# Optimization experiments

Measured on AMD Instinct MI355X. Metric: run time of the kernel, lower is better.

Reference implementation:

```python
import jax, jax.numpy as jnp
import numpy as np

EPS = 1e-5
TOP_K = 2


def setup_inputs() -> dict:
    key = jax.random.key(0)
    ks = jax.random.split(key, 6)
    T, H, F, E = 4096, 1024, 2816, 8
    scale = 0.02
    return {
        "hidden_states": jax.random.normal(ks[0], (T, H), dtype=jnp.float32),
        "ln_w": jnp.ones((H,), dtype=jnp.float32),
        "router_w": jax.random.normal(ks[1], (H, E), dtype=jnp.float32) * scale,
        "w_gate": jax.random.normal(ks[2], (E, H, F), dtype=jnp.float32) * scale,
        "w_up": jax.random.normal(ks[3], (E, H, F), dtype=jnp.float32) * scale,
        "w_down": jax.random.normal(ks[4], (E, F, H), dtype=jnp.float32) * scale,
    }


def reference(hidden_states, ln_w, router_w, w_gate, w_up, w_down):
    # RMSNorm (LlamaRMSNorm)
    var = jnp.mean(hidden_states * hidden_states, axis=-1, keepdims=True)
    x = hidden_states * jax.lax.rsqrt(var + EPS) * ln_w  # [T, H]

    # TopKRouter: softmax over experts, then top-k probs/indices
    logits = x @ router_w                     # [T, E]
    probs = jax.nn.softmax(logits, axis=-1)
    topk_p, topk_i = jax.lax.top_k(probs, TOP_K)  # [T, K]

    # Dense combine weights [T, E]: prob for routed experts, 0 otherwise
    T = x.shape[0]
    combine = jnp.zeros_like(probs).at[jnp.arange(T)[:, None], topk_i].add(topk_p)

    # Experts: Llama-style gated MLP (SwiGLU); loop over fixed small expert set
    out = jnp.zeros_like(x)
    for e in range(w_gate.shape[0]):
        h = jax.nn.silu(x @ w_gate[e]) * (x @ w_up[e])   # [T, F]
        out = out + combine[:, e:e + 1] * (h @ w_down[e])
    return out
```

## Files before the change

kernel.cpp:

```cpp
#include <hip/hip_runtime.h>

#define T_TOK 4096
#define H_DIM 1024
#define F_DIM 2816
#define E_NUM 8
#define EPSV 1e-5f

typedef unsigned short u16;
typedef __attribute__((ext_vector_type(8))) short bf16x8;
typedef __attribute__((ext_vector_type(4))) float f32x4;

__device__ __forceinline__ u16 f2bf(float f) {
  union { float f; unsigned u; } c; c.f = f;
  unsigned u = c.u;
  return (u16)((u + 0x7FFFu + ((u >> 16) & 1u)) >> 16);
}

__device__ __forceinline__ void llds16(const u16* g, u16* l) {
  __builtin_amdgcn_global_load_lds(
      (const __attribute__((address_space(1))) unsigned int*)g,
      (__attribute__((address_space(3))) unsigned int*)l, 16, 0, 0);
}

__global__ __launch_bounds__(256) void router_kernel(
    const float* __restrict__ hs, const float* __restrict__ lnw,
    const float* __restrict__ rw, u16* __restrict__ x_h,
    int* __restrict__ cnt, int* __restrict__ list,
    float* __restrict__ wcomb, int* __restrict__ slot) {
  const int wave = threadIdx.x >> 6;
  const int lane = threadIdx.x & 63;
  const int t = blockIdx.x * 4 + wave;
  const float* row = hs + (size_t)t * H_DIM;

  float4 v[4];
  float ss = 0.f;
#pragma unroll
  for (int j = 0; j < 4; ++j) {
    v[j] = ((const float4*)row)[j * 64 + lane];
    ss += v[j].x * v[j].x + v[j].y * v[j].y + v[j].z * v[j].z + v[j].w * v[j].w;
  }
#pragma unroll
  for (int m = 32; m; m >>= 1) ss += __shfl_xor(ss, m, 64);
  const float inv = rsqrtf(ss * (1.0f / H_DIM) + EPSV);

  float lg[E_NUM];
#pragma unroll
  for (int e = 0; e < E_NUM; ++e) lg[e] = 0.f;

#pragma unroll
  for (int j = 0; j < 4; ++j) {
    const int idx = j * 64 + lane;
    const int h0 = idx * 4;
    float4 w4 = ((const float4*)lnw)[idx];
    float xv[4] = {v[j].x * inv * w4.x, v[j].y * inv * w4.y,
                   v[j].z * inv * w4.z, v[j].w * inv * w4.w};
    ushort4 xs;
    xs.x = f2bf(xv[0]); xs.y = f2bf(xv[1]); xs.z = f2bf(xv[2]); xs.w = f2bf(xv[3]);
    ((ushort4*)(x_h + (size_t)t * H_DIM))[idx] = xs;
#pragma unroll
    for (int q = 0; q < 4; ++q) {
      const float* rr = rw + (size_t)(h0 + q) * E_NUM;
      float4 a = ((const float4*)rr)[0];
      float4 b = ((const float4*)rr)[1];
      lg[0] += xv[q] * a.x; lg[1] += xv[q] * a.y;
      lg[2] += xv[q] * a.z; lg[3] += xv[q] * a.w;
      lg[4] += xv[q] * b.x; lg[5] += xv[q] * b.y;
      lg[6] += xv[q] * b.z; lg[7] += xv[q] * b.w;
    }
  }
#pragma unroll
  for (int e = 0; e < E_NUM; ++e)
#pragma unroll
    for (int m = 32; m; m >>= 1) lg[e] += __shfl_xor(lg[e], m, 64);

  if (lane == 0) {
    float mx = lg[0];
#pragma unroll
    for (int e = 1; e < E_NUM; ++e) mx = fmaxf(mx, lg[e]);
    float p[E_NUM], s = 0.f;
#pragma unroll
    for (int e = 0; e < E_NUM; ++e) { p[e] = __expf(lg[e] - mx); s += p[e]; }
    const float invs = 1.0f / s;
    int e1 = 0; float b1 = p[0];
#pragma unroll
    for (int e = 1; e < E_NUM; ++e) if (p[e] > b1) { b1 = p[e]; e1 = e; }
    int e2 = -1; float b2 = -1.f;
#pragma unroll
    for (int e = 0; e < E_NUM; ++e) if (e != e1 && p[e] > b2) { b2 = p[e]; e2 = e; }
    b1 *= invs; b2 *= invs;
    int p1 = atomicAdd(&cnt[e1], 1);
    list[e1 * T_TOK + p1] = t; wcomb[e1 * T_TOK + p1] = b1;
    slot[2 * t] = (e1 << 16) | p1;
    int p2 = atomicAdd(&cnt[e2], 1);
    list[e2 * T_TOK + p2] = t; wcomb[e2 * T_TOK + p2] = b2;
    slot[2 * t + 1] = (e2 << 16) | p2;
  }
}

__global__ void offsets_kernel(const int* __restrict__ cnt, int* __restrict__ offs) {
  if (threadIdx.x == 0) {
    int s = 0;
    for (int e = 0; e < E_NUM; ++e) { offs[e] = s; s += cnt[e]; }
  }
}

__global__ __launch_bounds__(256) void transpose_cvt(
    const float* __restrict__ in, u16* __restrict__ out, int R, int C) {
  __shared__ float tile[32][33];
  const size_t base = (size_t)blockIdx.z * R * C;
  const int c0 = blockIdx.x * 32, r0 = blockIdx.y * 32;
  const int tx = threadIdx.x, ty = threadIdx.y;
#pragma unroll
  for (int j = 0; j < 32; j += 8)
    tile[ty + j][tx] = in[base + (size_t)(r0 + ty + j) * C + c0 + tx];
  __syncthreads();
#pragma unroll
  for (int j = 0; j < 32; j += 8)
    out[base + (size_t)(c0 + ty + j) * R + r0 + tx] = f2bf(tile[tx][ty + j]);
}

__global__ __launch_bounds__(256) void gemm1_kernel(
    const u16* __restrict__ x_h, const u16* __restrict__ wgT,
    const u16* __restrict__ wuT, const int* __restrict__ cnt,
    const int* __restrict__ offs, const int* __restrict__ list,
    u16* __restrict__ hbuf) {
  const int e = blockIdx.z;
  const int n_e = cnt[e];
  const int rt = blockIdx.y;
  if (rt * 128 >= n_e) return;
  const int ft = blockIdx.x;

  __shared__ __align__(16) u16 As[128 * 64];
  __shared__ __align__(16) u16 Bgs[64 * 64];
  __shared__ __align__(16) u16 Bus[64 * 64];
  __shared__ int tok[128];

  const int tid = threadIdx.x;
  if (tid < 128) {
    int r = rt * 128 + tid;
    if (r >= n_e) r = n_e - 1;
    tok[tid] = list[e * T_TOK + r];
  }
  __syncthreads();

  const int wv = tid >> 6, lane = tid & 63;
  const int wm = wv >> 1, wn = wv & 1;
  const int lrow = lane & 15, quad = lane >> 4;
  const int srow = lane >> 3, schunk = lane & 7;

  const u16* agp[4];
#pragma unroll
  for (int i = 0; i < 4; ++i) {
    int r = wv * 32 + i * 8 + srow;
    agp[i] = x_h + (size_t)tok[r] * H_DIM + ((schunk ^ (r & 7)) << 3);
  }
  const size_t wb = ((size_t)e * F_DIM + (size_t)ft * 64) * H_DIM;
  const u16* bgp[2]; const u16* bup[2];
#pragma unroll
  for (int i = 0; i < 2; ++i) {
    int r = wv * 16 + i * 8 + srow;
    size_t g = wb + (size_t)r * H_DIM + ((schunk ^ (r & 7)) << 3);
    bgp[i] = wgT + g;
    bup[i] = wuT + g;
  }

  const u16* aptr[4][2]; const u16* bgptr[2][2]; const u16* buptr[2][2];
#pragma unroll
  for (int tm = 0; tm < 4; ++tm) {
    int row = wm * 64 + tm * 16 + lrow;
#pragma unroll
    for (int ks = 0; ks < 2; ++ks)
      aptr[tm][ks] = &As[row * 64 + (((ks * 4 + quad) ^ (row & 7)) << 3)];
  }
#pragma unroll
  for (int tn = 0; tn < 2; ++tn) {
    int row = wn * 32 + tn * 16 + lrow;
#pragma unroll
    for (int ks = 0; ks < 2; ++ks) {
      int off = row * 64 + (((ks * 4 + quad) ^ (row & 7)) << 3);
      bgptr[tn][ks] = &Bgs[off];
      buptr[tn][ks] = &Bus[off];
    }
  }

  f32x4 accg[4][2], accu[4][2];
#pragma unroll
  for (int i = 0; i < 4; ++i)
#pragma unroll
    for (int j = 0; j < 2; ++j) {
      accg[i][j] = f32x4{0.f, 0.f, 0.f, 0.f};
      accu[i][j] = f32x4{0.f, 0.f, 0.f, 0.f};
    }

  for (int k0 = 0; k0 < H_DIM; k0 += 64) {
#pragma unroll
    for (int i = 0; i < 4; ++i)
      llds16(agp[i] + k0, &As[(wv * 32 + i * 8) * 64]);
#pragma unroll
    for (int i = 0; i < 2; ++i) {
      llds16(bgp[i] + k0, &Bgs[(wv * 16 + i * 8) * 64]);
      llds16(bup[i] + k0, &Bus[(wv * 16 + i * 8) * 64]);
    }
    __syncthreads();
#pragma unroll
    for (int ks = 0; ks < 2; ++ks) {
      bf16x8 a[4], bg[2], bu[2];
#pragma unroll
      for (int tm = 0; tm < 4; ++tm) a[tm] = *(const bf16x8*)aptr[tm][ks];
#pragma unroll
      for (int tn = 0; tn < 2; ++tn) {
        bg[tn] = *(const bf16x8*)bgptr[tn][ks];
        bu[tn] = *(const bf16x8*)buptr[tn][ks];
      }
#pragma unroll
      for (int tm = 0; tm < 4; ++tm)
#pragma unroll
        for (int tn = 0; tn < 2; ++tn) {
          accg[tm][tn] = __builtin_amdgcn_mfma_f32_16x16x32_bf16(a[tm], bg[tn], accg[tm][tn], 0, 0, 0);
          accu[tm][tn] = __builtin_amdgcn_mfma_f32_16x16x32_bf16(a[tm], bu[tn], accu[tm][tn], 0, 0, 0);
        }
    }
    __syncthreads();
  }

  const int oe = offs[e];
#pragma unroll
  for (int tm = 0; tm < 4; ++tm) {
    const int lr0 = wm * 64 + tm * 16 + quad * 4;
#pragma unroll
    for (int rr = 0; rr < 4; ++rr) {
      const int gr = rt * 128 + lr0 + rr;
      if (gr < n_e) {
#pragma unroll
        for (int tn = 0; tn < 2; ++tn) {
          float g = accg[tm][tn][rr];
          float u = accu[tm][tn][rr];
          float hv = g / (1.0f + __expf(-g)) * u;
          int col = ft * 64 + wn * 32 + tn * 16 + lrow;
          hbuf[(size_t)(oe + gr) * F_DIM + col] = f2bf(hv);
        }
      }
    }
  }
}

__global__ __launch_bounds__(256) void gemm2_kernel(
    const u16* __restrict__ hbuf, const u16* __restrict__ wdT,
    const int* __restrict__ cnt, const int* __restrict__ offs,
    const float* __restrict__ wcomb, float* __restrict__ contrib) {
  const int e = blockIdx.z;
  const int n_e = cnt[e];
  const int rt = blockIdx.y;
  if (rt * 128 >= n_e) return;
  const int nt = blockIdx.x;

  __shared__ __align__(16) u16 As[128 * 64];
  __shared__ __align__(16) u16 Bs[128 * 64];
  __shared__ int hrow[128];

  const int tid = threadIdx.x;
  const int oe = offs[e];
  if (tid < 128) {
    int r = rt * 128 + tid;
    if (r >= n_e) r = n_e - 1;
    hrow[tid] = oe + r;
  }
  __syncthreads();

  const int wv = tid >> 6, lane = tid & 63;
  const int wm = wv >> 1, wn = wv & 1;
  const int lrow = lane & 15, quad = lane >> 4;
  const int srow = lane >> 3, schunk = lane & 7;

  const u16* agp[4];
#pragma unroll
  for (int i = 0; i < 4; ++i) {
    int r = wv * 32 + i * 8 + srow;
    agp[i] = hbuf + (size_t)hrow[r] * F_DIM + ((schunk ^ (r & 7)) << 3);
  }
  const size_t wb = ((size_t)e * H_DIM + (size_t)nt * 128) * F_DIM;
  const u16* bgp[4];
#pragma unroll
  for (int i = 0; i < 4; ++i) {
    int r = wv * 32 + i * 8 + srow;
    bgp[i] = wdT + wb + (size_t)r * F_DIM + ((schunk ^ (r & 7)) << 3);
  }

  const u16* aptr[4][2]; const u16* bptr[4][2];
#pragma unroll
  for (int tm = 0; tm < 4; ++tm) {
    int row = wm * 64 + tm * 16 + lrow;
#pragma unroll
    for (int ks = 0; ks < 2; ++ks)
      aptr[tm][ks] = &As[row * 64 + (((ks * 4 + quad) ^ (row & 7)) << 3)];
  }
#pragma unroll
  for (int tn = 0; tn < 4; ++tn) {
    int row = wn * 64 + tn * 16 + lrow;
#pragma unroll
    for (int ks = 0; ks < 2; ++ks)
      bptr[tn][ks] = &Bs[row * 64 + (((ks * 4 + quad) ^ (row & 7)) << 3)];
  }

  f32x4 acc[4][4];
#pragma unroll
  for (int i = 0; i < 4; ++i)
#pragma unroll
    for (int j = 0; j < 4; ++j) acc[i][j] = f32x4{0.f, 0.f, 0.f, 0.f};

  for (int k0 = 0; k0 < F_DIM; k0 += 64) {
#pragma unroll
    for (int i = 0; i < 4; ++i) {
      llds16(agp[i] + k0, &As[(wv * 32 + i * 8) * 64]);
      llds16(bgp[i] + k0, &Bs[(wv * 32 + i * 8) * 64]);
    }
    __syncthreads();
#pragma unroll
    for (int ks = 0; ks < 2; ++ks) {
      bf16x8 a[4], b[4];
#pragma unroll
      for (int tm = 0; tm < 4; ++tm) a[tm] = *(const bf16x8*)aptr[tm][ks];
#pragma unroll
      for (int tn = 0; tn < 4; ++tn) b[tn] = *(const bf16x8*)bptr[tn][ks];
#pragma unroll
      for (int tm = 0; tm < 4; ++tm)
#pragma unroll
        for (int tn = 0; tn < 4; ++tn)
          acc[tm][tn] = __builtin_amdgcn_mfma_f32_16x16x32_bf16(a[tm], b[tn], acc[tm][tn], 0, 0, 0);
    }
    __syncthreads();
  }

#pragma unroll
  for (int tm = 0; tm < 4; ++tm) {
    const int lr0 = wm * 64 + tm * 16 + quad * 4;
#pragma unroll
    for (int rr = 0; rr < 4; ++rr) {
      const int gr = rt * 128 + lr0 + rr;
      if (gr < n_e) {
        const float cw = wcomb[e * T_TOK + gr];
#pragma unroll
        for (int tn = 0; tn < 4; ++tn) {
          int col = nt * 128 + wn * 64 + tn * 16 + lrow;
          contrib[(size_t)(oe + gr) * H_DIM + col] = acc[tm][tn][rr] * cw;
        }
      }
    }
  }
}

__global__ __launch_bounds__(256) void combine_kernel(
    const float* __restrict__ contrib, const int* __restrict__ offs,
    const int* __restrict__ slot, float* __restrict__ out) {
  const int t = blockIdx.x;
  const int s0 = slot[2 * t], s1 = slot[2 * t + 1];
  const int r0 = offs[s0 >> 16] + (s0 & 0xFFFF);
  const int r1 = offs[s1 >> 16] + (s1 & 0xFFFF);
  float4 a = ((const float4*)(contrib + (size_t)r0 * H_DIM))[threadIdx.x];
  float4 b = ((const float4*)(contrib + (size_t)r1 * H_DIM))[threadIdx.x];
  float4 o = {a.x + b.x, a.y + b.y, a.z + b.z, a.w + b.w};
  ((float4*)(out + (size_t)t * H_DIM))[threadIdx.x] = o;
}

extern "C" void kernel_launch(void* const* d_in, const int* in_sizes, int n_in,
                              void* d_out, int out_size, void* d_ws, size_t ws_size,
                              hipStream_t stream) {
  const float* hs  = (const float*)d_in[0];
  const float* lnw = (const float*)d_in[1];
  const float* rw  = (const float*)d_in[2];
  const float* wg  = (const float*)d_in[3];
  const float* wu  = (const float*)d_in[4];
  const float* wd  = (const float*)d_in[5];
  float* out = (float*)d_out;

  char* p = (char*)d_ws;
  const size_t SZ_XH = (size_t)T_TOK * H_DIM * 2;
  const size_t SZ_W  = (size_t)E_NUM * F_DIM * H_DIM * 2;
  const size_t SZ_HB = (size_t)T_TOK * 2 * F_DIM * 2;
  const size_t SZ_CT = (size_t)T_TOK * 2 * H_DIM * 4;

  u16* x_h  = (u16*)p;   p += SZ_XH;
  u16* wgT  = (u16*)p;   p += SZ_W;
  u16* wuT  = (u16*)p;   p += SZ_W;
  u16* wdT  = (u16*)p;   p += SZ_W;
  u16* hbuf = (u16*)p;   p += SZ_HB;
  float* contrib = (float*)p; p += SZ_CT;
  int* cnt  = (int*)p;   p += 256;
  int* offs = (int*)p;   p += 256;
  int* list = (int*)p;   p += (size_t)E_NUM * T_TOK * 4;
  float* wcomb = (float*)p; p += (size_t)E_NUM * T_TOK * 4;
  int* slot = (int*)p;   p += (size_t)T_TOK * 2 * 4;

  hipMemsetAsync(cnt, 0, 256, stream);
  router_kernel<<<T_TOK / 4, 256, 0, stream>>>(hs, lnw, rw, x_h, cnt, list, wcomb, slot);
  offsets_kernel<<<1, 64, 0, stream>>>(cnt, offs);
  transpose_cvt<<<dim3(F_DIM / 32, H_DIM / 32, E_NUM), dim3(32, 8), 0, stream>>>(wg, wgT, H_DIM, F_DIM);
  transpose_cvt<<<dim3(F_DIM / 32, H_DIM / 32, E_NUM), dim3(32, 8), 0, stream>>>(wu, wuT, H_DIM, F_DIM);
  transpose_cvt<<<dim3(H_DIM / 32, F_DIM / 32, E_NUM), dim3(32, 8), 0, stream>>>(wd, wdT, F_DIM, H_DIM);
  gemm1_kernel<<<dim3(F_DIM / 64, T_TOK / 128, E_NUM), 256, 0, stream>>>(x_h, wgT, wuT, cnt, offs, list, hbuf);
  gemm2_kernel<<<dim3(H_DIM / 128, T_TOK / 128, E_NUM), 256, 0, stream>>>(hbuf, wdT, cnt, offs, wcomb, contrib);
  combine_kernel<<<T_TOK, 256, 0, stream>>>(contrib, offs, slot, out);
}
```

Baseline: 652.8 us.

## Double-buffer GEMM LDS loads, fuse weight transposes, atomically scatter expert outputs

Both expert GEMMs now double-buffer their LDS tiles. The next k-slice is issued via global_load_lds before computing the current one, with explicit vmcnt waits and raw barriers, so memory latency overlaps MFMA work. The three weight transpose launches become a single kernel with 128x32 tiles and vectorised float4 reads and ushort4 writes. The contrib buffer and combine kernel are removed: gemm2 atomically adds weighted results directly into a zeroed output. This adds float atomics, whose summation order is nondeterministic, plus a memset of the output. It also doubles LDS use per block, which may lower occupancy.

```diff
diff --git a/kernel.cpp b/kernel.cpp
--- a/kernel.cpp
+++ b/kernel.cpp
@@ -26,7 +26,7 @@
     const float* __restrict__ hs, const float* __restrict__ lnw,
     const float* __restrict__ rw, u16* __restrict__ x_h,
     int* __restrict__ cnt, int* __restrict__ list,
-    float* __restrict__ wcomb, int* __restrict__ slot) {
+    float* __restrict__ wcomb) {
   const int wave = threadIdx.x >> 6;
   const int lane = threadIdx.x & 63;
   const int t = blockIdx.x * 4 + wave;
@@ -90,10 +90,8 @@
     b1 *= invs; b2 *= invs;
     int p1 = atomicAdd(&cnt[e1], 1);
     list[e1 * T_TOK + p1] = t; wcomb[e1 * T_TOK + p1] = b1;
-    slot[2 * t] = (e1 << 16) | p1;
     int p2 = atomicAdd(&cnt[e2], 1);
     list[e2 * T_TOK + p2] = t; wcomb[e2 * T_TOK + p2] = b2;
-    slot[2 * t + 1] = (e2 << 16) | p2;
   }
 }
 
@@ -104,19 +102,46 @@
   }
 }
 
-__global__ __launch_bounds__(256) void transpose_cvt(
-    const float* __restrict__ in, u16* __restrict__ out, int R, int C) {
-  __shared__ float tile[32][33];
-  const size_t base = (size_t)blockIdx.z * R * C;
-  const int c0 = blockIdx.x * 32, r0 = blockIdx.y * 32;
-  const int tx = threadIdx.x, ty = threadIdx.y;
-#pragma unroll
-  for (int j = 0; j < 32; j += 8)
-    tile[ty + j][tx] = in[base + (size_t)(r0 + ty + j) * C + c0 + tx];
+#define TPW 5632
+__global__ __launch_bounds__(256) void transpose_cvt_all(
+    const float* __restrict__ wg, const float* __restrict__ wu,
+    const float* __restrict__ wd, u16* __restrict__ wgT,
+    u16* __restrict__ wuT, u16* __restrict__ wdT) {
+  __shared__ float tile[128][37];
+  const int bx = blockIdx.x;
+  const int which = bx / TPW;
+  const int rem = bx - which * TPW;
+  const int e = rem / 704;
+  const int t = rem - e * 704;
+  const float* in; u16* outp; int R, C, rt, ct;
+  if (which == 0)      { in = wg; outp = wgT; R = H_DIM; C = F_DIM; rt = t / 88; ct = t - rt * 88; }
+  else if (which == 1) { in = wu; outp = wuT; R = H_DIM; C = F_DIM; rt = t / 88; ct = t - rt * 88; }
+  else                 { in = wd; outp = wdT; R = F_DIM; C = H_DIM; rt = t >> 5; ct = t & 31; }
+  const size_t base = (size_t)e * R * C;
+  const int r0 = rt * 128, c0 = ct * 32;
+  const int tid = threadIdx.x;
+
+  const int rr = tid >> 3, cq = tid & 7;
+#pragma unroll
+  for (int i = 0; i < 4; ++i) {
+    float4 v = *(const float4*)(in + base + (size_t)(r0 + rr + 32 * i) * C + c0 + cq * 4);
+    float* dst = &tile[rr + 32 * i][cq * 4];
+    dst[0] = v.x; dst[1] = v.y; dst[2] = v.z; dst[3] = v.w;
+  }
   __syncthreads();
-#pragma unroll
-  for (int j = 0; j < 32; j += 8)
-    out[base + (size_t)(c0 + ty + j) * R + r0 + tx] = f2bf(tile[tx][ty + j]);
+
+  const int cc = tid >> 4, rq0 = tid & 15;
+#pragma unroll
+  for (int jj = 0; jj < 4; ++jj) {
+    const int c = cc + 16 * (jj & 1);
+    const int rq = rq0 + 16 * (jj >> 1);
+    ushort4 o;
+    o.x = f2bf(tile[rq * 4 + 0][c]);
+    o.y = f2bf(tile[rq * 4 + 1][c]);
+    o.z = f2bf(tile[rq * 4 + 2][c]);
+    o.w = f2bf(tile[rq * 4 + 3][c]);
+    *(ushort4*)(outp + base + (size_t)(c0 + c) * R + r0 + rq * 4) = o;
+  }
 }
 
 __global__ __launch_bounds__(256) void gemm1_kernel(
@@ -130,19 +155,11 @@
   if (rt * 128 >= n_e) return;
   const int ft = blockIdx.x;
 
-  __shared__ __align__(16) u16 As[128 * 64];
-  __shared__ __align__(16) u16 Bgs[64 * 64];
-  __shared__ __align__(16) u16 Bus[64 * 64];
-  __shared__ int tok[128];
+  __shared__ __align__(16) u16 As[2][128 * 64];
+  __shared__ __align__(16) u16 Bgs[2][64 * 64];
+  __shared__ __align__(16) u16 Bus[2][64 * 64];
 
   const int tid = threadIdx.x;
-  if (tid < 128) {
-    int r = rt * 128 + tid;
-    if (r >= n_e) r = n_e - 1;
-    tok[tid] = list[e * T_TOK + r];
-  }
-  __syncthreads();
-
   const int wv = tid >> 6, lane = tid & 63;
   const int wm = wv >> 1, wn = wv & 1;
   const int lrow = lane & 15, quad = lane >> 4;
@@ -151,36 +168,35 @@
   const u16* agp[4];
 #pragma unroll
   for (int i = 0; i < 4; ++i) {
-    int r = wv * 32 + i * 8 + srow;
-    agp[i] = x_h + (size_t)tok[r] * H_DIM + ((schunk ^ (r & 7)) << 3);
+    const int rl = wv * 32 + i * 8 + srow;
+    int gr = rt * 128 + rl; if (gr >= n_e) gr = n_e - 1;
+    const int tkn = list[e * T_TOK + gr];
+    agp[i] = x_h + (size_t)tkn * H_DIM + ((schunk ^ (rl & 7)) << 3);
   }
   const size_t wb = ((size_t)e * F_DIM + (size_t)ft * 64) * H_DIM;
   const u16* bgp[2]; const u16* bup[2];
 #pragma unroll
   for (int i = 0; i < 2; ++i) {
-    int r = wv * 16 + i * 8 + srow;
-    size_t g = wb + (size_t)r * H_DIM + ((schunk ^ (r & 7)) << 3);
+    const int r = wv * 16 + i * 8 + srow;
+    const size_t g = wb + (size_t)r * H_DIM + ((schunk ^ (r & 7)) << 3);
     bgp[i] = wgT + g;
     bup[i] = wuT + g;
   }
 
-  const u16* aptr[4][2]; const u16* bgptr[2][2]; const u16* buptr[2][2];
+  int aoff[4][2], boff[2][2];
 #pragma unroll
   for (int tm = 0; tm < 4; ++tm) {
-    int row = wm * 64 + tm * 16 + lrow;
+    const int row = wm * 64 + tm * 16 + lrow;
 #pragma unroll
     for (int ks = 0; ks < 2; ++ks)
-      aptr[tm][ks] = &As[row * 64 + (((ks * 4 + quad) ^ (row & 7)) << 3)];
+      aoff[tm][ks] = row * 64 + (((ks * 4 + quad) ^ (row & 7)) << 3);
   }
 #pragma unroll
   for (int tn = 0; tn < 2; ++tn) {
-    int row = wn * 32 + tn * 16 + lrow;
-#pragma unroll
-    for (int ks = 0; ks < 2; ++ks) {
-      int off = row * 64 + (((ks * 4 + quad) ^ (row & 7)) << 3);
-      bgptr[tn][ks] = &Bgs[off];
-      buptr[tn][ks] = &Bus[off];
-    }
+    const int row = wn * 32 + tn * 16 + lrow;
+#pragma unroll
+    for (int ks = 0; ks < 2; ++ks)
+      boff[tn][ks] = row * 64 + (((ks * 4 + quad) ^ (row & 7)) << 3);
   }
 
   f32x4 accg[4][2], accu[4][2];
@@ -192,25 +208,26 @@
       accu[i][j] = f32x4{0.f, 0.f, 0.f, 0.f};
     }
 
-  for (int k0 = 0; k0 < H_DIM; k0 += 64) {
+  auto stage = [&](int b, int k0) {
 #pragma unroll
     for (int i = 0; i < 4; ++i)
-      llds16(agp[i] + k0, &As[(wv * 32 + i * 8) * 64]);
+      llds16(agp[i] + k0, &As[b][(wv * 32 + i * 8) * 64]);
 #pragma unroll
     for (int i = 0; i < 2; ++i) {
-      llds16(bgp[i] + k0, &Bgs[(wv * 16 + i * 8) * 64]);
-      llds16(bup[i] + k0, &Bus[(wv * 16 + i * 8) * 64]);
-    }
-    __syncthreads();
+      llds16(bgp[i] + k0, &Bgs[b][(wv * 16 + i * 8) * 64]);
+      llds16(bup[i] + k0, &Bus[b][(wv * 16 + i * 8) * 64]);
+    }
+  };
+  auto compute = [&](int b) {
 #pragma unroll
     for (int ks = 0; ks < 2; ++ks) {
       bf16x8 a[4], bg[2], bu[2];
 #pragma unroll
-      for (int tm = 0; tm < 4; ++tm) a[tm] = *(const bf16x8*)aptr[tm][ks];
+      for (int tm = 0; tm < 4; ++tm) a[tm] = *(const bf16x8*)&As[b][aoff[tm][ks]];
 #pragma unroll
       for (int tn = 0; tn < 2; ++tn) {
-        bg[tn] = *(const bf16x8*)bgptr[tn][ks];
-        bu[tn] = *(const bf16x8*)buptr[tn][ks];
+        bg[tn] = *(const bf16x8*)&Bgs[b][boff[tn][ks]];
+        bu[tn] = *(const bf16x8*)&Bus[b][boff[tn][ks]];
       }
 #pragma unroll
       for (int tm = 0; tm < 4; ++tm)
@@ -220,7 +237,31 @@
           accu[tm][tn] = __builtin_amdgcn_mfma_f32_16x16x32_bf16(a[tm], bu[tn], accu[tm][tn], 0, 0, 0);
         }
     }
-    __syncthreads();
+  };
+
+  stage(0, 0);
+#pragma unroll 1
+  for (int k0 = 0; k0 < H_DIM; k0 += 128) {
+    const bool s1 = (k0 + 64) < H_DIM;
+    if (s1) {
+      stage(1, k0 + 64);
+      asm volatile("s_waitcnt vmcnt(8)" ::: "memory");
+    } else {
+      asm volatile("s_waitcnt vmcnt(0)" ::: "memory");
+    }
+    __builtin_amdgcn_s_barrier();
+    compute(0);
+    __builtin_amdgcn_s_barrier();
+    const bool s2 = (k0 + 128) < H_DIM;
+    if (s2) {
+      stage(0, k0 + 128);
+      asm volatile("s_waitcnt vmcnt(8)" ::: "memory");
+    } else {
+      asm volatile("s_waitcnt vmcnt(0)" ::: "memory");
+    }
+    __builtin_amdgcn_s_barrier();
+    compute(1);
+    __builtin_amdgcn_s_barrier();
   }
 
   const int oe = offs[e];
@@ -247,26 +288,19 @@
 __global__ __launch_bounds__(256) void gemm2_kernel(
     const u16* __restrict__ hbuf, const u16* __restrict__ wdT,
     const int* __restrict__ cnt, const int* __restrict__ offs,
-    const float* __restrict__ wcomb, float* __restrict__ contrib) {
+    const float* __restrict__ wcomb, const int* __restrict__ list,
+    float* __restrict__ out) {
   const int e = blockIdx.z;
   const int n_e = cnt[e];
   const int rt = blockIdx.y;
   if (rt * 128 >= n_e) return;
   const int nt = blockIdx.x;
 
-  __shared__ __align__(16) u16 As[128 * 64];
-  __shared__ __align__(16) u16 Bs[128 * 64];
-  __shared__ int hrow[128];
+  __shared__ __align__(16) u16 As[2][128 * 64];
+  __shared__ __align__(16) u16 Bs[2][128 * 64];
 
   const int tid = threadIdx.x;
   const int oe = offs[e];
-  if (tid < 128) {
-    int r = rt * 128 + tid;
-    if (r >= n_e) r = n_e - 1;
-    hrow[tid] = oe + r;
-  }
-  __syncthreads();
-
   const int wv = tid >> 6, lane = tid & 63;
   const int wm = wv >> 1, wn = wv & 1;
   const int lrow = lane & 15, quad = lane >> 4;
@@ -275,31 +309,32 @@
   const u16* agp[4];
 #pragma unroll
   for (int i = 0; i < 4; ++i) {
-    int r = wv * 32 + i * 8 + srow;
-    agp[i] = hbuf + (size_t)hrow[r] * F_DIM + ((schunk ^ (r & 7)) << 3);
+    const int rl = wv * 32 + i * 8 + srow;
+    int gr = rt * 128 + rl; if (gr >= n_e) gr = n_e - 1;
+    agp[i] = hbuf + (size_t)(oe + gr) * F_DIM + ((schunk ^ (rl & 7)) << 3);
   }
   const size_t wb = ((size_t)e * H_DIM + (size_t)nt * 128) * F_DIM;
   const u16* bgp[4];
 #pragma unroll
   for (int i = 0; i < 4; ++i) {
-    int r = wv * 32 + i * 8 + srow;
+    const int r = wv * 32 + i * 8 + srow;
     bgp[i] = wdT + wb + (size_t)r * F_DIM + ((schunk ^ (r & 7)) << 3);
   }
 
-  const u16* aptr[4][2]; const u16* bptr[4][2];
+  int aoff[4][2], boff[4][2];
 #pragma unroll
   for (int tm = 0; tm < 4; ++tm) {
-    int row = wm * 64 + tm * 16 + lrow;
+    const int row = wm * 64 + tm * 16 + lrow;
 #pragma unroll
     for (int ks = 0; ks < 2; ++ks)
-      aptr[tm][ks] = &As[row * 64 + (((ks * 4 + quad) ^ (row & 7)) << 3)];
+      aoff[tm][ks] = row * 64 + (((ks * 4 + quad) ^ (row & 7)) << 3);
   }
 #pragma unroll
   for (int tn = 0; tn < 4; ++tn) {
-    int row = wn * 64 + tn * 16 + lrow;
+    const int row = wn * 64 + tn * 16 + lrow;
 #pragma unroll
     for (int ks = 0; ks < 2; ++ks)
-      bptr[tn][ks] = &Bs[row * 64 + (((ks * 4 + quad) ^ (row & 7)) << 3)];
+      boff[tn][ks] = row * 64 + (((ks * 4 + quad) ^ (row & 7)) << 3);
   }
 
   f32x4 acc[4][4];
@@ -308,27 +343,52 @@
 #pragma unroll
     for (int j = 0; j < 4; ++j) acc[i][j] = f32x4{0.f, 0.f, 0.f, 0.f};
 
-  for (int k0 = 0; k0 < F_DIM; k0 += 64) {
+  auto stage = [&](int b, int k0) {
 #pragma unroll
     for (int i = 0; i < 4; ++i) {
-      llds16(agp[i] + k0, &As[(wv * 32 + i * 8) * 64]);
-      llds16(bgp[i] + k0, &Bs[(wv * 32 + i * 8) * 64]);
-    }
-    __syncthreads();
+      llds16(agp[i] + k0, &As[b][(wv * 32 + i * 8) * 64]);
+      llds16(bgp[i] + k0, &Bs[b][(wv * 32 + i * 8) * 64]);
+    }
+  };
+  auto compute = [&](int b) {
 #pragma unroll
     for (int ks = 0; ks < 2; ++ks) {
-      bf16x8 a[4], b[4];
-#pragma unroll
-      for (int tm = 0; tm < 4; ++tm) a[tm] = *(const bf16x8*)aptr[tm][ks];
-#pragma unroll
-      for (int tn = 0; tn < 4; ++tn) b[tn] = *(const bf16x8*)bptr[tn][ks];
+      bf16x8 a[4], bb[4];
+#pragma unroll
+      for (int tm = 0; tm < 4; ++tm) a[tm] = *(const bf16x8*)&As[b][aoff[tm][ks]];
+#pragma unroll
+      for (int tn = 0; tn < 4; ++tn) bb[tn] = *(const bf16x8*)&Bs[b][boff[tn][ks]];
 #pragma unroll
       for (int tm = 0; tm < 4; ++tm)
 #pragma unroll
         for (int tn = 0; tn < 4; ++tn)
-          acc[tm][tn] = __builtin_amdgcn_mfma_f32_16x16x32_bf16(a[tm], b[tn], acc[tm][tn], 0, 0, 0);
-    }
-    __syncthreads();
+          acc[tm][tn] = __builtin_amdgcn_mfma_f32_16x16x32_bf16(a[tm], bb[tn], acc[tm][tn], 0, 0, 0);
+    }
+  };
+
+  stage(0, 0);
+#pragma unroll 1
+  for (int k0 = 0; k0 < F_DIM; k0 += 128) {
+    const bool s1 = (k0 + 64) < F_DIM;
+    if (s1) {
+      stage(1, k0 + 64);
+      asm volatile("s_waitcnt vmcnt(8)" ::: "memory");
+    } else {
+      asm volatile("s_waitcnt vmcnt(0)" ::: "memory");
+    }
+    __builtin_amdgcn_s_barrier();
+    compute(0);
+    __builtin_amdgcn_s_barrier();
+    const bool s2 = (k0 + 128) < F_DIM;
+    if (s2) {
+      stage(0, k0 + 128);
+      asm volatile("s_waitcnt vmcnt(8)" ::: "memory");
+    } else {
+      asm volatile("s_waitcnt vmcnt(0)" ::: "memory");
+    }
+    __builtin_amdgcn_s_barrier();
+    compute(1);
+    __builtin_amdgcn_s_barrier();
   }
 
 #pragma unroll
@@ -339,27 +399,15 @@
       const int gr = rt * 128 + lr0 + rr;
       if (gr < n_e) {
         const float cw = wcomb[e * T_TOK + gr];
+        const int tkn = list[e * T_TOK + gr];
 #pragma unroll
         for (int tn = 0; tn < 4; ++tn) {
-          int col = nt * 128 + wn * 64 + tn * 16 + lrow;
-          contrib[(size_t)(oe + gr) * H_DIM + col] = acc[tm][tn][rr] * cw;
+          const int col = nt * 128 + wn * 64 + tn * 16 + lrow;
+          atomicAdd(&out[(size_t)tkn * H_DIM + col], acc[tm][tn][rr] * cw);
         }
       }
     }
   }
-}
-
-__global__ __launch_bounds__(256) void combine_kernel(
-    const float* __restrict__ contrib, const int* __restrict__ offs,
-    const int* __restrict__ slot, float* __restrict__ out) {
-  const int t = blockIdx.x;
-  const int s0 = slot[2 * t], s1 = slot[2 * t + 1];
-  const int r0 = offs[s0 >> 16] + (s0 & 0xFFFF);
-  const int r1 = offs[s1 >> 16] + (s1 & 0xFFFF);
-  float4 a = ((const float4*)(contrib + (size_t)r0 * H_DIM))[threadIdx.x];
-  float4 b = ((const float4*)(contrib + (size_t)r1 * H_DIM))[threadIdx.x];
-  float4 o = {a.x + b.x, a.y + b.y, a.z + b.z, a.w + b.w};
-  ((float4*)(out + (size_t)t * H_DIM))[threadIdx.x] = o;
 }
 
 extern "C" void kernel_launch(void* const* d_in, const int* in_sizes, int n_in,
@@ -377,27 +425,22 @@
   const size_t SZ_XH = (size_t)T_TOK * H_DIM * 2;
   const size_t SZ_W  = (size_t)E_NUM * F_DIM * H_DIM * 2;
   const size_t SZ_HB = (size_t)T_TOK * 2 * F_DIM * 2;
-  const size_t SZ_CT = (size_t)T_TOK * 2 * H_DIM * 4;
 
   u16* x_h  = (u16*)p;   p += SZ_XH;
   u16* wgT  = (u16*)p;   p += SZ_W;
   u16* wuT  = (u16*)p;   p += SZ_W;
   u16* wdT  = (u16*)p;   p += SZ_W;
   u16* hbuf = (u16*)p;   p += SZ_HB;
-  float* contrib = (float*)p; p += SZ_CT;
   int* cnt  = (int*)p;   p += 256;
   int* offs = (int*)p;   p += 256;
   int* list = (int*)p;   p += (size_t)E_NUM * T_TOK * 4;
   float* wcomb = (float*)p; p += (size_t)E_NUM * T_TOK * 4;
-  int* slot = (int*)p;   p += (size_t)T_TOK * 2 * 4;
 
   hipMemsetAsync(cnt, 0, 256, stream);
-  router_kernel<<<T_TOK / 4, 256, 0, stream>>>(hs, lnw, rw, x_h, cnt, list, wcomb, slot);
+  hipMemsetAsync(out, 0, (size_t)T_TOK * H_DIM * 4, stream);
+  router_kernel<<<T_TOK / 4, 256, 0, stream>>>(hs, lnw, rw, x_h, cnt, list, wcomb);
   offsets_kernel<<<1, 64, 0, stream>>>(cnt, offs);
-  transpose_cvt<<<dim3(F_DIM / 32, H_DIM / 32, E_NUM), dim3(32, 8), 0, stream>>>(wg, wgT, H_DIM, F_DIM);
-  transpose_cvt<<<dim3(F_DIM / 32, H_DIM / 32, E_NUM), dim3(32, 8), 0, stream>>>(wu, wuT, H_DIM, F_DIM);
-  transpose_cvt<<<dim3(H_DIM / 32, F_DIM / 32, E_NUM), dim3(32, 8), 0, stream>>>(wd, wdT, F_DIM, H_DIM);
+  transpose_cvt_all<<<3 * TPW, 256, 0, stream>>>(wg, wu, wd, wgT, wuT, wdT);
   gemm1_kernel<<<dim3(F_DIM / 64, T_TOK / 128, E_NUM), 256, 0, stream>>>(x_h, wgT, wuT, cnt, offs, list, hbuf);
-  gemm2_kernel<<<dim3(H_DIM / 128, T_TOK / 128, E_NUM), 256, 0, stream>>>(hbuf, wdT, cnt, offs, wcomb, contrib);
-  combine_kernel<<<T_TOK, 256, 0, stream>>>(contrib, offs, slot, out);
-}
+  gemm2_kernel<<<dim3(H_DIM / 128, T_TOK / 128, E_NUM), 256, 0, stream>>>(hbuf, wdT, cnt, offs, wcomb, list, out);
+}
```

After: 669.3 us. +2.5%, slower.
